# Kernel optimization log

Measured on AMD Instinct MI355X. Metric: run time of the kernel, lower is better.

Reference implementation:

```python
import jax, jax.numpy as jnp
import numpy as np

D = 256      # input channels
DK = 64      # key/query/value channels
BS, W, H = 8, 64, 64


def setup_inputs() -> dict:
    key = jax.random.key(0)
    k1, k2, k3, k4 = jax.random.split(key, 4)
    v = jax.random.normal(k1, (BS, D, W, H), dtype=jnp.float32)
    # conv1x1 weights collapse to plain matrices over the channel dim
    Wqkv = jax.random.normal(k2, (3 * DK, D), dtype=jnp.float32) * 0.02
    Wout = jax.random.normal(k3, (D, DK), dtype=jnp.float32) * 0.02
    gamma = jax.random.normal(k4, (1,), dtype=jnp.float32)  # original inits to 0; nonzero for a non-degenerate baseline
    return {"v": v, "Wqkv": Wqkv, "Wout": Wout, "gamma": gamma}


def reference(v, Wqkv, Wout, gamma):
    bs, c, w, h = v.shape
    n = w * h
    d_k = Wout.shape[1]
    x = v.reshape(bs, c, n)                      # (b, c, n)
    qkv = jnp.einsum('oc,bcn->bon', Wqkv, x)      # 1x1 conv == channel matmul
    q = qkv[:, :d_k]                              # (b, dk, n)
    k = qkv[:, d_k:2 * d_k]
    val = qkv[:, 2 * d_k:]
    s = jnp.einsum('bdi,bdj->bij', q, k)          # (b, n, n) = query^T key
    beta = jax.nn.softmax(s, axis=2)              # exp(s - logsumexp(s, axis=2))
    y = jnp.einsum('bdi,bij->bdj', val, beta)     # bmm(value, beta)
    o = jnp.einsum('od,bdn->bon', Wout, y) * gamma[0] + x
    return o.reshape(bs, c, w, h)
```

## Files before the change

kernel.cpp:

```cpp
#include <hip/hip_runtime.h>

typedef unsigned short ushort_t;
typedef __bf16 bf16x8 __attribute__((ext_vector_type(8)));
typedef short short4v __attribute__((ext_vector_type(4)));
typedef float f32x4 __attribute__((ext_vector_type(4)));
typedef unsigned int uint4v __attribute__((ext_vector_type(4)));
typedef unsigned int uint2v __attribute__((ext_vector_type(2)));

#define NTOK 4096
#define DMODEL 256
#define DK 64
#define BS 8
#define LN2INV 1.44269504088896f

__device__ __forceinline__ ushort_t f2bf(float f) {
  unsigned u = __builtin_bit_cast(unsigned, f);
  u += 0x7fffu + ((u >> 16) & 1u);
  return (ushort_t)(u >> 16);
}
__device__ __forceinline__ float bf2f(ushort_t s) {
  return __builtin_bit_cast(float, ((unsigned)s) << 16);
}
__device__ __forceinline__ bf16x8 lds_frag(const ushort_t* p) {
  return __builtin_bit_cast(bf16x8, *(const uint4v*)p);
}
__device__ __forceinline__ float fexp2(float x) {
#if __has_builtin(__builtin_amdgcn_exp2f)
  return __builtin_amdgcn_exp2f(x);
#else
  return exp2f(x);
#endif
}
__device__ __forceinline__ unsigned bfpack(float x, float y) {
  return __builtin_amdgcn_perm(__builtin_bit_cast(unsigned, y),
                               __builtin_bit_cast(unsigned, x), 0x07060302u);
}
__device__ __forceinline__ f32x4 mfma16(short4v a, short4v b, f32x4 c) {
#if defined(__HIP_DEVICE_COMPILE__)
#if __has_builtin(__builtin_amdgcn_mfma_f32_16x16x16bf16_1k)
  return __builtin_amdgcn_mfma_f32_16x16x16bf16_1k(a, b, c, 0, 0, 0);
#else
  typedef __bf16 bf16x4 __attribute__((ext_vector_type(4)));
  return __builtin_amdgcn_mfma_f32_16x16x16_bf16(__builtin_bit_cast(bf16x4, a),
                                                 __builtin_bit_cast(bf16x4, b), c, 0, 0, 0);
#endif
#else
  (void)a; (void)b;
  return c;
#endif
}

__global__ __launch_bounds__(256) void k_convert(const float* __restrict__ Wqkv,
                                                 const float* __restrict__ Wout,
                                                 ushort_t* __restrict__ Wb,
                                                 ushort_t* __restrict__ Woutb) {
  int i = blockIdx.x * 256 + threadIdx.x;
  if (i < 3 * DK * DMODEL) {
    float w = Wqkv[i];
    if (i < DK * DMODEL) w *= LN2INV;
    Wb[i] = f2bf(w);
  } else {
    int j = i - 3 * DK * DMODEL;
    Woutb[j] = f2bf(Wout[j]);
  }
}

__global__ __launch_bounds__(256) void k_transpose(const float* __restrict__ x,
                                                   ushort_t* __restrict__ xT) {
  const int b = blockIdx.z;
  const int c0 = blockIdx.y * 64;
  const int n0 = blockIdx.x * 64;
  const int tid = threadIdx.x;
  __shared__ __align__(16) ushort_t t[64 * 72];
  const float* xb = x + (size_t)b * DMODEL * NTOK;
  ushort_t* xTb = xT + (size_t)b * NTOK * DMODEL;
#pragma unroll
  for (int kr = 0; kr < 2; kr++) {
    int s = tid + 256 * kr;
    int c = s >> 3, ns = (s & 7) * 8;
    const float* src = xb + (size_t)(c0 + c) * NTOK + n0 + ns;
    f32x4 a = *(const f32x4*)src;
    f32x4 bq = *(const f32x4*)(src + 4);
    uint4v o;
    o.x = (unsigned)f2bf(a[0]) | ((unsigned)f2bf(a[1]) << 16);
    o.y = (unsigned)f2bf(a[2]) | ((unsigned)f2bf(a[3]) << 16);
    o.z = (unsigned)f2bf(bq[0]) | ((unsigned)f2bf(bq[1]) << 16);
    o.w = (unsigned)f2bf(bq[2]) | ((unsigned)f2bf(bq[3]) << 16);
    *(uint4v*)(t + c * 72 + ns) = o;
  }
  __syncthreads();
#pragma unroll
  for (int kr = 0; kr < 2; kr++) {
    int s = tid + 256 * kr;
    int n = s >> 3, cs = (s & 7) * 8;
    unsigned e0 = t[(cs + 0) * 72 + n], e1 = t[(cs + 1) * 72 + n];
    unsigned e2 = t[(cs + 2) * 72 + n], e3 = t[(cs + 3) * 72 + n];
    unsigned e4 = t[(cs + 4) * 72 + n], e5 = t[(cs + 5) * 72 + n];
    unsigned e6 = t[(cs + 6) * 72 + n], e7 = t[(cs + 7) * 72 + n];
    uint4v o;
    o.x = e0 | (e1 << 16); o.y = e2 | (e3 << 16);
    o.z = e4 | (e5 << 16); o.w = e6 | (e7 << 16);
    *(uint4v*)(xTb + (size_t)(n0 + n) * DMODEL + c0 + cs) = o;
  }
}

__global__ __launch_bounds__(256) void k_qkv(const ushort_t* __restrict__ xT,
                                             const ushort_t* __restrict__ W,
                                             ushort_t* __restrict__ QT,
                                             ushort_t* __restrict__ KT,
                                             ushort_t* __restrict__ Vv) {
  const int b = blockIdx.y;
  const int n0 = blockIdx.x * 64;
  const int tid = threadIdx.x;
  const int lane = tid & 63, wv = tid >> 6;
  const int quad = lane >> 4, l15 = lane & 15;
  __shared__ __align__(16) ushort_t lw[192 * 40];
  __shared__ __align__(16) ushort_t lx[64 * 40];
  f32x4 acc[3][4];
  const f32x4 zero4 = {0.f, 0.f, 0.f, 0.f};
#pragma unroll
  for (int i = 0; i < 3; i++)
#pragma unroll
    for (int j = 0; j < 4; j++) acc[i][j] = zero4;

  const ushort_t* xTb = xT + ((size_t)b * NTOK + n0) * DMODEL;

  for (int c0 = 0; c0 < DMODEL; c0 += 32) {
    __syncthreads();
#pragma unroll
    for (int kr = 0; kr < 3; kr++) {
      int s = tid + 256 * kr;
      int o = s >> 2, cs = (s & 3) * 8;
      *(uint4v*)(lw + o * 40 + cs) = *(const uint4v*)(W + o * DMODEL + c0 + cs);
    }
    {
      int n = tid >> 2, cs = (tid & 3) * 8;
      *(uint4v*)(lx + n * 40 + cs) = *(const uint4v*)(xTb + (size_t)n * DMODEL + c0 + cs);
    }
    __syncthreads();
    bf16x8 bb[4];
#pragma unroll
    for (int nt = 0; nt < 4; nt++) bb[nt] = lds_frag(lx + (nt * 16 + l15) * 40 + quad * 8);
#pragma unroll
    for (int mt = 0; mt < 3; mt++) {
      bf16x8 a = lds_frag(lw + (wv * 48 + mt * 16 + l15) * 40 + quad * 8);
#pragma unroll
      for (int nt = 0; nt < 4; nt++)
        acc[mt][nt] = __builtin_amdgcn_mfma_f32_16x16x32_bf16(a, bb[nt], acc[mt][nt], 0, 0, 0);
    }
  }
#pragma unroll
  for (int mt = 0; mt < 3; mt++) {
    int o = wv * 48 + mt * 16 + quad * 4;
#pragma unroll
    for (int nt = 0; nt < 4; nt++) {
      int n = n0 + nt * 16 + l15;
      f32x4 v4 = acc[mt][nt];
      if (o < 128) {
        ushort_t* dst = (o < 64) ? (QT + ((size_t)b * NTOK + n) * DK + o)
                                 : (KT + ((size_t)b * NTOK + n) * DK + (o - 64));
        uint2v ww;
        ww.x = (unsigned)f2bf(v4[0]) | ((unsigned)f2bf(v4[1]) << 16);
        ww.y = (unsigned)f2bf(v4[2]) | ((unsigned)f2bf(v4[3]) << 16);
        *(uint2v*)dst = ww;
      } else {
        int d = o - 128;
#pragma unroll
        for (int r = 0; r < 4; r++)
          Vv[((size_t)b * DK + d + r) * NTOK + n] = f2bf(v4[r]);
      }
    }
  }
}

__global__ __launch_bounds__(256) void k_rsum(const ushort_t* __restrict__ QT,
                                              const ushort_t* __restrict__ KT,
                                              float* __restrict__ Rp) {
  const int id = blockIdx.x;
  const int b = id & 7;
  const int rest = id >> 3;
  const int i0 = (rest & 63) * 64;
  const int jh = rest >> 6;
  const int tid = threadIdx.x;
  const int lane = tid & 63, wv = tid >> 6;
  const int quad = lane >> 4, l15 = lane & 15;
  __shared__ __align__(16) ushort_t lq[64 * 72];
  __shared__ __align__(16) ushort_t lk[2][64 * 72];
  const ushort_t* QTb = QT + ((size_t)b * NTOK + i0) * DK;
  const ushort_t* KTb = KT + ((size_t)b * NTOK + jh * 2048) * DK;
#pragma unroll
  for (int kr = 0; kr < 2; kr++) {
    int s = tid + 256 * kr;
    int row = s >> 3, ds = (s & 7) * 8;
    *(uint4v*)(lq + row * 72 + ds) = *(const uint4v*)(QTb + (size_t)row * DK + ds);
    *(uint4v*)(lk[0] + row * 72 + ds) = *(const uint4v*)(KTb + (size_t)row * DK + ds);
  }
  __syncthreads();
  bf16x8 a0 = lds_frag(lq + (wv * 16 + l15) * 72 + quad * 8);
  bf16x8 a1 = lds_frag(lq + (wv * 16 + l15) * 72 + 32 + quad * 8);
  float lsum0 = 0.f, lsum1 = 0.f, lsum2 = 0.f, lsum3 = 0.f;
  const f32x4 zero4 = {0.f, 0.f, 0.f, 0.f};
  for (int it = 0; it < 32; it++) {
    if (it + 1 < 32) {
      const ushort_t* src = KTb + (size_t)(it + 1) * 64 * DK;
      ushort_t* dstb = lk[(it + 1) & 1];
#pragma unroll
      for (int kr = 0; kr < 2; kr++) {
        int s = tid + 256 * kr;
        int row = s >> 3, ds = (s & 7) * 8;
        *(uint4v*)(dstb + row * 72 + ds) = *(const uint4v*)(src + (size_t)row * DK + ds);
      }
    }
    const ushort_t* kb = lk[it & 1];
#pragma unroll
    for (int nt = 0; nt < 4; nt++) {
      bf16x8 b0 = lds_frag(kb + (nt * 16 + l15) * 72 + quad * 8);
      bf16x8 b1 = lds_frag(kb + (nt * 16 + l15) * 72 + 32 + quad * 8);
      f32x4 s4 = __builtin_amdgcn_mfma_f32_16x16x32_bf16(a0, b0, zero4, 0, 0, 0);
      s4 = __builtin_amdgcn_mfma_f32_16x16x32_bf16(a1, b1, s4, 0, 0, 0);
      lsum0 += fexp2(s4[0]);
      lsum1 += fexp2(s4[1]);
      lsum2 += fexp2(s4[2]);
      lsum3 += fexp2(s4[3]);
    }
    __syncthreads();
  }
#pragma unroll
  for (int off = 1; off < 16; off <<= 1) {
    lsum0 += __shfl_xor(lsum0, off);
    lsum1 += __shfl_xor(lsum1, off);
    lsum2 += __shfl_xor(lsum2, off);
    lsum3 += __shfl_xor(lsum3, off);
  }
  if (l15 < 4) {
    float v = (l15 == 0) ? lsum0 : (l15 == 1) ? lsum1 : (l15 == 2) ? lsum2 : lsum3;
    Rp[((size_t)(jh * 8 + b)) * NTOK + i0 + wv * 16 + quad * 4 + l15] = v;
  }
}

__global__ __launch_bounds__(256) void k_rmerge(const float* __restrict__ Rp,
                                                float* __restrict__ Rr) {
  int g = blockIdx.x * 256 + threadIdx.x;
  Rr[g] = 1.0f / (Rp[g] + Rp[BS * NTOK + g]);
}

__global__ __launch_bounds__(256) void k_pv(const ushort_t* __restrict__ QT,
                                            const ushort_t* __restrict__ KT,
                                            const ushort_t* __restrict__ Vv,
                                            const float* __restrict__ Rr,
                                            ushort_t* __restrict__ Yp) {
  const int id = blockIdx.x;
  const int b = id & 7;
  const int rest = id >> 3;
  const int j0 = (rest & 63) * 64;
  const int ih = rest >> 6;
  const int tid = threadIdx.x;
  const int lane = tid & 63, wv = tid >> 6;
  const int quad = lane >> 4, l15 = lane & 15;

  __shared__ __align__(16) ushort_t pool[18432];
#define LQ(buf) (pool + (buf) * 4608)
#define LV(buf) (pool + 9216 + (buf) * 4608)
  float* rbuf = (float*)pool;
  ushort_t* pbuf = pool + 8704;

  const ushort_t* KTb = KT + ((size_t)b * NTOK + j0) * DK;
  const ushort_t* QTb = QT + ((size_t)b * NTOK + ih * 2048) * DK;
  const ushort_t* Vbb = Vv + (size_t)b * DK * NTOK + ih * 2048;
  const float* Rrb = Rr + (size_t)b * NTOK + ih * 2048;

#pragma unroll
  for (int kr = 0; kr < 2; kr++) {
    int s = tid + 256 * kr;
    int row = s >> 3, ds = (s & 7) * 8;
    *(uint4v*)(LQ(0) + row * 72 + ds) = *(const uint4v*)(KTb + (size_t)row * DK + ds);
  }
  __syncthreads();
  bf16x8 kb0[4], kb1[4];
#pragma unroll
  for (int nt = 0; nt < 4; nt++) {
    kb0[nt] = lds_frag(LQ(0) + (nt * 16 + l15) * 72 + quad * 8);
    kb1[nt] = lds_frag(LQ(0) + (nt * 16 + l15) * 72 + 32 + quad * 8);
  }
  __syncthreads();
#pragma unroll
  for (int kr = 0; kr < 2; kr++) {
    int s = tid + 256 * kr;
    int row = s >> 3, ds = (s & 7) * 8;
    *(uint4v*)(LQ(0) + row * 72 + ds) = *(const uint4v*)(QTb + (size_t)row * DK + ds);
    *(uint4v*)(LV(0) + row * 72 + ds) = *(const uint4v*)(Vbb + (size_t)row * NTOK + ds);
  }
  __syncthreads();

  const f32x4 zero4 = {0.f, 0.f, 0.f, 0.f};
  f32x4 yt[4][4];
#pragma unroll
  for (int i = 0; i < 4; i++)
#pragma unroll
    for (int j = 0; j < 4; j++) yt[i][j] = zero4;

  for (int it = 0; it < 32; it++) {
    const int cb = it & 1, nb = cb ^ 1;
    f32x4 rv = *(const f32x4*)(Rrb + it * 64 + wv * 16 + quad * 4);
    if (it + 1 < 32) {
      const ushort_t* qsrc = QTb + (size_t)(it + 1) * 64 * DK;
#pragma unroll
      for (int kr = 0; kr < 2; kr++) {
        int s = tid + 256 * kr;
        int row = s >> 3, ds = (s & 7) * 8;
        *(uint4v*)(LQ(nb) + row * 72 + ds) = *(const uint4v*)(qsrc + (size_t)row * DK + ds);
        *(uint4v*)(LV(nb) + row * 72 + ds) =
            *(const uint4v*)(Vbb + (size_t)row * NTOK + (it + 1) * 64 + ds);
      }
    }
    bf16x8 a0 = lds_frag(LQ(cb) + (wv * 16 + l15) * 72 + quad * 8);
    bf16x8 a1 = lds_frag(LQ(cb) + (wv * 16 + l15) * 72 + 32 + quad * 8);
    short4v vf[4];
#pragma unroll
    for (int dsub = 0; dsub < 4; dsub++)
      vf[dsub] = __builtin_bit_cast(short4v,
          *(const uint2v*)(LV(cb) + (dsub * 16 + l15) * 72 + wv * 16 + quad * 4));
#pragma unroll
    for (int nt = 0; nt < 4; nt++) {
      f32x4 s4 = __builtin_amdgcn_mfma_f32_16x16x32_bf16(a0, kb0[nt], zero4, 0, 0, 0);
      s4 = __builtin_amdgcn_mfma_f32_16x16x32_bf16(a1, kb1[nt], s4, 0, 0, 0);
      uint2v wp;
      wp.x = bfpack(fexp2(s4[0]) * rv[0], fexp2(s4[1]) * rv[1]);
      wp.y = bfpack(fexp2(s4[2]) * rv[2], fexp2(s4[3]) * rv[3]);
      short4v wf = __builtin_bit_cast(short4v, wp);
#pragma unroll
      for (int dsub = 0; dsub < 4; dsub++)
        yt[nt][dsub] = mfma16(wf, vf[dsub], yt[nt][dsub]);
    }
    __syncthreads();
  }

  if (wv == 0) {
#pragma unroll
    for (int nt = 0; nt < 4; nt++)
#pragma unroll
      for (int dsub = 0; dsub < 4; dsub++)
        *(f32x4*)(rbuf + (dsub * 16 + l15) * 68 + nt * 16 + quad * 4) = yt[nt][dsub];
  }
  __syncthreads();
  if (wv == 1) {
#pragma unroll
    for (int nt = 0; nt < 4; nt++)
#pragma unroll
      for (int dsub = 0; dsub < 4; dsub++) {
        float* p = rbuf + (dsub * 16 + l15) * 68 + nt * 16 + quad * 4;
        *(f32x4*)p = *(const f32x4*)p + yt[nt][dsub];
      }
  }
  __syncthreads();
  if (wv == 2) {
#pragma unroll
    for (int nt = 0; nt < 4; nt++)
#pragma unroll
      for (int dsub = 0; dsub < 4; dsub++) {
        float* p = rbuf + (dsub * 16 + l15) * 68 + nt * 16 + quad * 4;
        *(f32x4*)p = *(const f32x4*)p + yt[nt][dsub];
      }
  }
  __syncthreads();
  if (wv == 3) {
#pragma unroll
    for (int nt = 0; nt < 4; nt++)
#pragma unroll
      for (int dsub = 0; dsub < 4; dsub++) {
        const float* p = rbuf + (dsub * 16 + l15) * 68 + nt * 16 + quad * 4;
        f32x4 v4 = *(const f32x4*)p + yt[nt][dsub];
#pragma unroll
        for (int r = 0; r < 4; r++)
          pbuf[(nt * 16 + quad * 4 + r) * 72 + dsub * 16 + l15] = f2bf(v4[r]);
      }
  }
  __syncthreads();

  ushort_t* Ypb = Yp + ((size_t)(ih * 8 + b) * NTOK + j0) * DK;
#pragma unroll
  for (int kr = 0; kr < 2; kr++) {
    int s = tid + 256 * kr;
    int row = s >> 3, c8 = (s & 7) * 8;
    *(uint4v*)(Ypb + (size_t)row * DK + c8) = *(const uint4v*)(pbuf + row * 72 + c8);
  }
#undef LQ
#undef LV
}

__global__ __launch_bounds__(256) void k_out(const ushort_t* __restrict__ Yp,
                                             const ushort_t* __restrict__ Wout,
                                             const float* __restrict__ gammap,
                                             const float* __restrict__ x,
                                             float* __restrict__ outp) {
  const int id = blockIdx.x;
  const int b = id & 7;
  const int n0 = (id >> 3) * 64;
  const int tid = threadIdx.x;
  const int lane = tid & 63, wv = tid >> 6;
  const int quad = lane >> 4, l15 = lane & 15;
  __shared__ __align__(16) ushort_t pbuf[64 * 72];

  const ushort_t* Y0 = Yp + ((size_t)b * NTOK + n0) * DK;
  const ushort_t* Y1 = Yp + ((size_t)(8 + b) * NTOK + n0) * DK;
#pragma unroll
  for (int kr = 0; kr < 2; kr++) {
    int s = tid + 256 * kr;
    int row = s >> 3, c8 = (s & 7) * 8;
    uint4v ua = *(const uint4v*)(Y0 + (size_t)row * DK + c8);
    uint4v ub = *(const uint4v*)(Y1 + (size_t)row * DK + c8);
    uint4v oc;
    unsigned* pa = (unsigned*)&ua;
    unsigned* pb = (unsigned*)&ub;
    unsigned* po = (unsigned*)&oc;
#pragma unroll
    for (int w = 0; w < 4; w++) {
      float lo = bf2f((ushort_t)(pa[w] & 0xffff)) + bf2f((ushort_t)(pb[w] & 0xffff));
      float hi = bf2f((ushort_t)(pa[w] >> 16)) + bf2f((ushort_t)(pb[w] >> 16));
      po[w] = bfpack(lo, hi);
    }
    *(uint4v*)(pbuf + row * 72 + c8) = oc;
  }
  __syncthreads();

  const f32x4 zero4 = {0.f, 0.f, 0.f, 0.f};
  bf16x8 yb0[4], yb1[4];
#pragma unroll
  for (int nt = 0; nt < 4; nt++) {
    yb0[nt] = lds_frag(pbuf + (nt * 16 + l15) * 72 + quad * 8);
    yb1[nt] = lds_frag(pbuf + (nt * 16 + l15) * 72 + 32 + quad * 8);
  }
  f32x4 oacc[4][4];
#pragma unroll
  for (int m = 0; m < 4; m++)
#pragma unroll
    for (int nt = 0; nt < 4; nt++) oacc[m][nt] = zero4;
#pragma unroll
  for (int m = 0; m < 4; m++) {
    int c = (wv * 4 + m) * 16 + l15;
    bf16x8 aw0 = __builtin_bit_cast(bf16x8, *(const uint4v*)(Wout + c * DK + quad * 8));
    bf16x8 aw1 = __builtin_bit_cast(bf16x8, *(const uint4v*)(Wout + c * DK + 32 + quad * 8));
#pragma unroll
    for (int nt = 0; nt < 4; nt++) {
      oacc[m][nt] = __builtin_amdgcn_mfma_f32_16x16x32_bf16(aw0, yb0[nt], oacc[m][nt], 0, 0, 0);
      oacc[m][nt] = __builtin_amdgcn_mfma_f32_16x16x32_bf16(aw1, yb1[nt], oacc[m][nt], 0, 0, 0);
    }
  }
  float g = gammap[0];
  const float* xb = x + (size_t)b * DMODEL * NTOK;
  float* ob = outp + (size_t)b * DMODEL * NTOK;
#pragma unroll
  for (int m = 0; m < 4; m++) {
    int cbase = (wv * 4 + m) * 16 + quad * 4;
#pragma unroll
    for (int nt = 0; nt < 4; nt++) {
      int n = n0 + nt * 16 + l15;
#pragma unroll
      for (int r = 0; r < 4; r++) {
        size_t idx = (size_t)(cbase + r) * NTOK + n;
        ob[idx] = oacc[m][nt][r] * g + xb[idx];
      }
    }
  }
}

extern "C" void kernel_launch(void* const* d_in, const int* in_sizes, int n_in,
                              void* d_out, int out_size, void* d_ws, size_t ws_size,
                              hipStream_t stream) {
  const float* v = (const float*)d_in[0];
  const float* Wqkv = (const float*)d_in[1];
  const float* Wout = (const float*)d_in[2];
  const float* gamma = (const float*)d_in[3];
  float* outp = (float*)d_out;

  ushort_t* xT = (ushort_t*)d_ws;
  ushort_t* QT = xT + (size_t)BS * NTOK * DMODEL;
  ushort_t* KT = QT + (size_t)BS * NTOK * DK;
  ushort_t* Vs = KT + (size_t)BS * NTOK * DK;
  ushort_t* Wb = Vs + (size_t)BS * DK * NTOK;
  ushort_t* Woutb = Wb + 3 * DK * DMODEL;
  float* Rp = (float*)(Woutb + DMODEL * DK);
  float* Rr = Rp + 2 * (size_t)BS * NTOK;
  ushort_t* Yp = (ushort_t*)(Rr + (size_t)BS * NTOK);

  k_convert<<<dim3(256), 256, 0, stream>>>(Wqkv, Wout, Wb, Woutb);
  k_transpose<<<dim3(64, 4, BS), 256, 0, stream>>>(v, xT);
  k_qkv<<<dim3(64, BS), 256, 0, stream>>>(xT, Wb, QT, KT, Vs);
  k_rsum<<<dim3(1024), 256, 0, stream>>>(QT, KT, Rp);
  k_rmerge<<<dim3(128), 256, 0, stream>>>(Rp, Rr);
  k_pv<<<dim3(1024), 256, 0, stream>>>(QT, KT, Vs, Rr, Yp);
  k_out<<<dim3(512), 256, 0, stream>>>(Yp, Woutb, gamma, v, outp);
}
```

Measured before the change: 217.4 us.

## Load MFMA fragments directly from global memory and fold normalizer into exponent

The rsum and pv kernels stop staging Q, K and V tiles through LDS and instead load MFMA operand fragments straight from global memory into registers, double-buffered across iterations. This removes the per-iteration __syncthreads barriers and the LDS round trips. The merge kernel now stores -log2 of the row sum, and pv feeds it in as the MFMA accumulator init, so the normalization folds into the exp2 argument and the per-element multiply goes away. The cost is more register pressure and global loads that are less coalesced and repeated across waves, served mostly from cache.

```diff
diff --git a/kernel.cpp b/kernel.cpp
--- a/kernel.cpp
+++ b/kernel.cpp
@@ -23,6 +23,12 @@
 }
 __device__ __forceinline__ bf16x8 lds_frag(const ushort_t* p) {
   return __builtin_bit_cast(bf16x8, *(const uint4v*)p);
+}
+__device__ __forceinline__ bf16x8 ldg8(const ushort_t* p) {
+  return __builtin_bit_cast(bf16x8, *(const uint4v*)p);
+}
+__device__ __forceinline__ short4v ldg4(const ushort_t* p) {
+  return __builtin_bit_cast(short4v, *(const uint2v*)p);
 }
 __device__ __forceinline__ float fexp2(float x) {
 #if __has_builtin(__builtin_amdgcn_exp2f)
@@ -184,56 +190,57 @@
   const int tid = threadIdx.x;
   const int lane = tid & 63, wv = tid >> 6;
   const int quad = lane >> 4, l15 = lane & 15;
-  __shared__ __align__(16) ushort_t lq[64 * 72];
-  __shared__ __align__(16) ushort_t lk[2][64 * 72];
   const ushort_t* QTb = QT + ((size_t)b * NTOK + i0) * DK;
   const ushort_t* KTb = KT + ((size_t)b * NTOK + jh * 2048) * DK;
-#pragma unroll
-  for (int kr = 0; kr < 2; kr++) {
-    int s = tid + 256 * kr;
-    int row = s >> 3, ds = (s & 7) * 8;
-    *(uint4v*)(lq + row * 72 + ds) = *(const uint4v*)(QTb + (size_t)row * DK + ds);
-    *(uint4v*)(lk[0] + row * 72 + ds) = *(const uint4v*)(KTb + (size_t)row * DK + ds);
-  }
-  __syncthreads();
-  bf16x8 a0 = lds_frag(lq + (wv * 16 + l15) * 72 + quad * 8);
-  bf16x8 a1 = lds_frag(lq + (wv * 16 + l15) * 72 + 32 + quad * 8);
-  float lsum0 = 0.f, lsum1 = 0.f, lsum2 = 0.f, lsum3 = 0.f;
+
+  const int qoff = (wv * 16 + l15) * DK + quad * 8;
+  bf16x8 a0 = ldg8(QTb + qoff);
+  bf16x8 a1 = ldg8(QTb + qoff + 32);
+
+  const int koff = l15 * DK + quad * 8;
+  bf16x8 kb0[2][4], kb1[2][4];
+  float ls0 = 0.f, ls1 = 0.f, ls2 = 0.f, ls3 = 0.f;
   const f32x4 zero4 = {0.f, 0.f, 0.f, 0.f};
-  for (int it = 0; it < 32; it++) {
-    if (it + 1 < 32) {
-      const ushort_t* src = KTb + (size_t)(it + 1) * 64 * DK;
-      ushort_t* dstb = lk[(it + 1) & 1];
-#pragma unroll
-      for (int kr = 0; kr < 2; kr++) {
-        int s = tid + 256 * kr;
-        int row = s >> 3, ds = (s & 7) * 8;
-        *(uint4v*)(dstb + row * 72 + ds) = *(const uint4v*)(src + (size_t)row * DK + ds);
-      }
-    }
-    const ushort_t* kb = lk[it & 1];
-#pragma unroll
-    for (int nt = 0; nt < 4; nt++) {
-      bf16x8 b0 = lds_frag(kb + (nt * 16 + l15) * 72 + quad * 8);
-      bf16x8 b1 = lds_frag(kb + (nt * 16 + l15) * 72 + 32 + quad * 8);
-      f32x4 s4 = __builtin_amdgcn_mfma_f32_16x16x32_bf16(a0, b0, zero4, 0, 0, 0);
-      s4 = __builtin_amdgcn_mfma_f32_16x16x32_bf16(a1, b1, s4, 0, 0, 0);
-      lsum0 += fexp2(s4[0]);
-      lsum1 += fexp2(s4[1]);
-      lsum2 += fexp2(s4[2]);
-      lsum3 += fexp2(s4[3]);
-    }
-    __syncthreads();
-  }
+
+#define LOADK(bb, itv)                                                       \
+  {                                                                          \
+    _Pragma("unroll") for (int nt = 0; nt < 4; nt++) {                       \
+      const ushort_t* kp = KTb + (size_t)((itv)*64 + nt * 16) * DK + koff;   \
+      kb0[bb][nt] = ldg8(kp);                                                \
+      kb1[bb][nt] = ldg8(kp + 32);                                           \
+    }                                                                        \
+  }
+#define STEPK(bb)                                                            \
+  {                                                                          \
+    _Pragma("unroll") for (int nt = 0; nt < 4; nt++) {                       \
+      f32x4 s4 = __builtin_amdgcn_mfma_f32_16x16x32_bf16(a0, kb0[bb][nt], zero4, 0, 0, 0); \
+      s4 = __builtin_amdgcn_mfma_f32_16x16x32_bf16(a1, kb1[bb][nt], s4, 0, 0, 0);          \
+      ls0 += fexp2(s4[0]);                                                   \
+      ls1 += fexp2(s4[1]);                                                   \
+      ls2 += fexp2(s4[2]);                                                   \
+      ls3 += fexp2(s4[3]);                                                   \
+    }                                                                        \
+  }
+
+  LOADK(0, 0);
+  for (int it = 0; it < 32; it += 2) {
+    LOADK(1, it + 1);
+    STEPK(0);
+    if (it + 2 < 32) LOADK(0, it + 2);
+    STEPK(1);
+  }
+#undef LOADK
+#undef STEPK
+
 #pragma unroll
   for (int off = 1; off < 16; off <<= 1) {
-    lsum0 += __shfl_xor(lsum0, off);
-    lsum1 += __shfl_xor(lsum1, off);
-    lsum2 += __shfl_xor(lsum2, off);
-    lsum3 += __shfl_xor(lsum3, off);
+    ls0 += __shfl_xor(ls0, off);
+    ls1 += __shfl_xor(ls1, off);
+    ls2 += __shfl_xor(ls2, off);
+    ls3 += __shfl_xor(ls3, off);
   }
   if (l15 < 4) {
-    float v = (l15 == 0) ? lsum0 : (l15 == 1) ? lsum1 : (l15 == 2) ? lsum2 : lsum3;
+    float v = (l15 == 0) ? ls0 : (l15 == 1) ? ls1 : (l15 == 2) ? ls2 : ls3;
     Rp[((size_t)(jh * 8 + b)) * NTOK + i0 + wv * 16 + quad * 4 + l15] = v;
   }
 }
@@ -241,7 +248,8 @@
 __global__ __launch_bounds__(256) void k_rmerge(const float* __restrict__ Rp,
                                                 float* __restrict__ Rr) {
   int g = blockIdx.x * 256 + threadIdx.x;
-  Rr[g] = 1.0f / (Rp[g] + Rp[BS * NTOK + g]);
+  float s = Rp[g] + Rp[BS * NTOK + g];
+  Rr[g] = -__log2f(s);
 }
 
 __global__ __launch_bounds__(256) void k_pv(const ushort_t* __restrict__ QT,
@@ -258,9 +266,7 @@
   const int lane = tid & 63, wv = tid >> 6;
   const int quad = lane >> 4, l15 = lane & 15;
 
-  __shared__ __align__(16) ushort_t pool[18432];
-#define LQ(buf) (pool + (buf) * 4608)
-#define LV(buf) (pool + 9216 + (buf) * 4608)
+  __shared__ __align__(16) ushort_t pool[13312];
   float* rbuf = (float*)pool;
   ushort_t* pbuf = pool + 8704;
 
@@ -269,71 +275,60 @@
   const ushort_t* Vbb = Vv + (size_t)b * DK * NTOK + ih * 2048;
   const float* Rrb = Rr + (size_t)b * NTOK + ih * 2048;
 
-#pragma unroll
-  for (int kr = 0; kr < 2; kr++) {
-    int s = tid + 256 * kr;
-    int row = s >> 3, ds = (s & 7) * 8;
-    *(uint4v*)(LQ(0) + row * 72 + ds) = *(const uint4v*)(KTb + (size_t)row * DK + ds);
-  }
-  __syncthreads();
   bf16x8 kb0[4], kb1[4];
 #pragma unroll
   for (int nt = 0; nt < 4; nt++) {
-    kb0[nt] = lds_frag(LQ(0) + (nt * 16 + l15) * 72 + quad * 8);
-    kb1[nt] = lds_frag(LQ(0) + (nt * 16 + l15) * 72 + 32 + quad * 8);
-  }
-  __syncthreads();
-#pragma unroll
-  for (int kr = 0; kr < 2; kr++) {
-    int s = tid + 256 * kr;
-    int row = s >> 3, ds = (s & 7) * 8;
-    *(uint4v*)(LQ(0) + row * 72 + ds) = *(const uint4v*)(QTb + (size_t)row * DK + ds);
-    *(uint4v*)(LV(0) + row * 72 + ds) = *(const uint4v*)(Vbb + (size_t)row * NTOK + ds);
-  }
-  __syncthreads();
-
+    const ushort_t* kp = KTb + (size_t)(nt * 16 + l15) * DK + quad * 8;
+    kb0[nt] = ldg8(kp);
+    kb1[nt] = ldg8(kp + 32);
+  }
+
+  f32x4 yt[4][4];
   const f32x4 zero4 = {0.f, 0.f, 0.f, 0.f};
-  f32x4 yt[4][4];
 #pragma unroll
   for (int i = 0; i < 4; i++)
 #pragma unroll
     for (int j = 0; j < 4; j++) yt[i][j] = zero4;
 
-  for (int it = 0; it < 32; it++) {
-    const int cb = it & 1, nb = cb ^ 1;
-    f32x4 rv = *(const f32x4*)(Rrb + it * 64 + wv * 16 + quad * 4);
-    if (it + 1 < 32) {
-      const ushort_t* qsrc = QTb + (size_t)(it + 1) * 64 * DK;
-#pragma unroll
-      for (int kr = 0; kr < 2; kr++) {
-        int s = tid + 256 * kr;
-        int row = s >> 3, ds = (s & 7) * 8;
-        *(uint4v*)(LQ(nb) + row * 72 + ds) = *(const uint4v*)(qsrc + (size_t)row * DK + ds);
-        *(uint4v*)(LV(nb) + row * 72 + ds) =
-            *(const uint4v*)(Vbb + (size_t)row * NTOK + (it + 1) * 64 + ds);
-      }
-    }
-    bf16x8 a0 = lds_frag(LQ(cb) + (wv * 16 + l15) * 72 + quad * 8);
-    bf16x8 a1 = lds_frag(LQ(cb) + (wv * 16 + l15) * 72 + 32 + quad * 8);
-    short4v vf[4];
-#pragma unroll
-    for (int dsub = 0; dsub < 4; dsub++)
-      vf[dsub] = __builtin_bit_cast(short4v,
-          *(const uint2v*)(LV(cb) + (dsub * 16 + l15) * 72 + wv * 16 + quad * 4));
-#pragma unroll
-    for (int nt = 0; nt < 4; nt++) {
-      f32x4 s4 = __builtin_amdgcn_mfma_f32_16x16x32_bf16(a0, kb0[nt], zero4, 0, 0, 0);
-      s4 = __builtin_amdgcn_mfma_f32_16x16x32_bf16(a1, kb1[nt], s4, 0, 0, 0);
-      uint2v wp;
-      wp.x = bfpack(fexp2(s4[0]) * rv[0], fexp2(s4[1]) * rv[1]);
-      wp.y = bfpack(fexp2(s4[2]) * rv[2], fexp2(s4[3]) * rv[3]);
-      short4v wf = __builtin_bit_cast(short4v, wp);
-#pragma unroll
-      for (int dsub = 0; dsub < 4; dsub++)
-        yt[nt][dsub] = mfma16(wf, vf[dsub], yt[nt][dsub]);
-    }
-    __syncthreads();
-  }
+  const int qoff = (wv * 16 + l15) * DK + quad * 8;
+  const int voff = wv * 16 + quad * 4;
+
+  bf16x8 qa0[2], qa1[2];
+  short4v vf[2][4];
+  f32x4 lr[2];
+
+#define LOADT(bb, itv)                                                        \
+  {                                                                           \
+    const ushort_t* qp = QTb + (size_t)(itv)*64 * DK + qoff;                  \
+    qa0[bb] = ldg8(qp);                                                       \
+    qa1[bb] = ldg8(qp + 32);                                                  \
+    lr[bb] = *(const f32x4*)(Rrb + (itv)*64 + voff);                          \
+    _Pragma("unroll") for (int ds = 0; ds < 4; ds++)                          \
+        vf[bb][ds] = ldg4(Vbb + (size_t)(ds * 16 + l15) * NTOK + (itv)*64 + voff); \
+  }
+#define STEPT(bb)                                                             \
+  {                                                                           \
+    _Pragma("unroll") for (int nt = 0; nt < 4; nt++) {                        \
+      f32x4 s4 = __builtin_amdgcn_mfma_f32_16x16x32_bf16(qa0[bb], kb0[nt], lr[bb], 0, 0, 0); \
+      s4 = __builtin_amdgcn_mfma_f32_16x16x32_bf16(qa1[bb], kb1[nt], s4, 0, 0, 0);           \
+      uint2v wp;                                                              \
+      wp.x = bfpack(fexp2(s4[0]), fexp2(s4[1]));                              \
+      wp.y = bfpack(fexp2(s4[2]), fexp2(s4[3]));                              \
+      short4v wf = __builtin_bit_cast(short4v, wp);                           \
+      _Pragma("unroll") for (int ds = 0; ds < 4; ds++)                        \
+          yt[nt][ds] = mfma16(wf, vf[bb][ds], yt[nt][ds]);                    \
+    }                                                                         \
+  }
+
+  LOADT(0, 0);
+  for (int it = 0; it < 32; it += 2) {
+    LOADT(1, it + 1);
+    STEPT(0);
+    if (it + 2 < 32) LOADT(0, it + 2);
+    STEPT(1);
+  }
+#undef LOADT
+#undef STEPT
 
   if (wv == 0) {
 #pragma unroll
@@ -384,8 +379,6 @@
     int row = s >> 3, c8 = (s & 7) * 8;
     *(uint4v*)(Ypb + (size_t)row * DK + c8) = *(const uint4v*)(pbuf + row * 72 + c8);
   }
-#undef LQ
-#undef LV
 }
 
 __global__ __launch_bounds__(256) void k_out(const ushort_t* __restrict__ Yp,
```

After: 338.0 us. 1.55x slower.

## Register-stage global prefetch, load fragments directly, fold softmax normalizer into MFMA bias

Applied to the files above, without the earlier changes.

The double-buffered tile prefetch in the row-sum and PV kernels now loads into registers before the MFMA work and writes them to LDS only after it, so global latency overlaps compute rather than stalling on a direct global-to-LDS store. Q fragments in k_rsum and K fragments in k_pv are read straight from global memory, which drops an LDS round trip and a barrier. The reciprocal row sum becomes -log2(sum) and is passed as the MFMA accumulator's initial value, replacing four multiplies per score tile with a free add inside exp2. This adds register pressure for the staged values and assumes fragment rows match the per-row bias layout.

```diff
diff --git a/kernel.cpp b/kernel.cpp
--- a/kernel.cpp
+++ b/kernel.cpp
@@ -184,32 +184,30 @@
   const int tid = threadIdx.x;
   const int lane = tid & 63, wv = tid >> 6;
   const int quad = lane >> 4, l15 = lane & 15;
-  __shared__ __align__(16) ushort_t lq[64 * 72];
   __shared__ __align__(16) ushort_t lk[2][64 * 72];
   const ushort_t* QTb = QT + ((size_t)b * NTOK + i0) * DK;
   const ushort_t* KTb = KT + ((size_t)b * NTOK + jh * 2048) * DK;
-#pragma unroll
-  for (int kr = 0; kr < 2; kr++) {
-    int s = tid + 256 * kr;
-    int row = s >> 3, ds = (s & 7) * 8;
-    *(uint4v*)(lq + row * 72 + ds) = *(const uint4v*)(QTb + (size_t)row * DK + ds);
-    *(uint4v*)(lk[0] + row * 72 + ds) = *(const uint4v*)(KTb + (size_t)row * DK + ds);
-  }
-  __syncthreads();
-  bf16x8 a0 = lds_frag(lq + (wv * 16 + l15) * 72 + quad * 8);
-  bf16x8 a1 = lds_frag(lq + (wv * 16 + l15) * 72 + 32 + quad * 8);
-  float lsum0 = 0.f, lsum1 = 0.f, lsum2 = 0.f, lsum3 = 0.f;
+
+  const int qoff = (wv * 16 + l15) * DK + quad * 8;
+  bf16x8 a0 = __builtin_bit_cast(bf16x8, *(const uint4v*)(QTb + qoff));
+  bf16x8 a1 = __builtin_bit_cast(bf16x8, *(const uint4v*)(QTb + qoff + 32));
+
+  const int sr0 = tid >> 3, sr1 = sr0 + 32;
+  const int c8 = (tid & 7) * 8;
+
+  *(uint4v*)(lk[0] + sr0 * 72 + c8) = *(const uint4v*)(KTb + (size_t)sr0 * DK + c8);
+  *(uint4v*)(lk[0] + sr1 * 72 + c8) = *(const uint4v*)(KTb + (size_t)sr1 * DK + c8);
+  __syncthreads();
+
+  float ls0 = 0.f, ls1 = 0.f, ls2 = 0.f, ls3 = 0.f;
   const f32x4 zero4 = {0.f, 0.f, 0.f, 0.f};
+
   for (int it = 0; it < 32; it++) {
+    uint4v p0, p1;
     if (it + 1 < 32) {
       const ushort_t* src = KTb + (size_t)(it + 1) * 64 * DK;
-      ushort_t* dstb = lk[(it + 1) & 1];
-#pragma unroll
-      for (int kr = 0; kr < 2; kr++) {
-        int s = tid + 256 * kr;
-        int row = s >> 3, ds = (s & 7) * 8;
-        *(uint4v*)(dstb + row * 72 + ds) = *(const uint4v*)(src + (size_t)row * DK + ds);
-      }
+      p0 = *(const uint4v*)(src + (size_t)sr0 * DK + c8);
+      p1 = *(const uint4v*)(src + (size_t)sr1 * DK + c8);
     }
     const ushort_t* kb = lk[it & 1];
 #pragma unroll
@@ -218,22 +216,28 @@
       bf16x8 b1 = lds_frag(kb + (nt * 16 + l15) * 72 + 32 + quad * 8);
       f32x4 s4 = __builtin_amdgcn_mfma_f32_16x16x32_bf16(a0, b0, zero4, 0, 0, 0);
       s4 = __builtin_amdgcn_mfma_f32_16x16x32_bf16(a1, b1, s4, 0, 0, 0);
-      lsum0 += fexp2(s4[0]);
-      lsum1 += fexp2(s4[1]);
-      lsum2 += fexp2(s4[2]);
-      lsum3 += fexp2(s4[3]);
+      ls0 += fexp2(s4[0]);
+      ls1 += fexp2(s4[1]);
+      ls2 += fexp2(s4[2]);
+      ls3 += fexp2(s4[3]);
+    }
+    if (it + 1 < 32) {
+      ushort_t* dstb = lk[(it + 1) & 1];
+      *(uint4v*)(dstb + sr0 * 72 + c8) = p0;
+      *(uint4v*)(dstb + sr1 * 72 + c8) = p1;
     }
     __syncthreads();
   }
+
 #pragma unroll
   for (int off = 1; off < 16; off <<= 1) {
-    lsum0 += __shfl_xor(lsum0, off);
-    lsum1 += __shfl_xor(lsum1, off);
-    lsum2 += __shfl_xor(lsum2, off);
-    lsum3 += __shfl_xor(lsum3, off);
+    ls0 += __shfl_xor(ls0, off);
+    ls1 += __shfl_xor(ls1, off);
+    ls2 += __shfl_xor(ls2, off);
+    ls3 += __shfl_xor(ls3, off);
   }
   if (l15 < 4) {
-    float v = (l15 == 0) ? lsum0 : (l15 == 1) ? lsum1 : (l15 == 2) ? lsum2 : lsum3;
+    float v = (l15 == 0) ? ls0 : (l15 == 1) ? ls1 : (l15 == 2) ? ls2 : ls3;
     Rp[((size_t)(jh * 8 + b)) * NTOK + i0 + wv * 16 + quad * 4 + l15] = v;
   }
 }
@@ -241,7 +245,8 @@
 __global__ __launch_bounds__(256) void k_rmerge(const float* __restrict__ Rp,
                                                 float* __restrict__ Rr) {
   int g = blockIdx.x * 256 + threadIdx.x;
-  Rr[g] = 1.0f / (Rp[g] + Rp[BS * NTOK + g]);
+  float s = Rp[g] + Rp[BS * NTOK + g];
+  Rr[g] = -__log2f(s);
 }
 
 __global__ __launch_bounds__(256) void k_pv(const ushort_t* __restrict__ QT,
@@ -269,31 +274,25 @@
   const ushort_t* Vbb = Vv + (size_t)b * DK * NTOK + ih * 2048;
   const float* Rrb = Rr + (size_t)b * NTOK + ih * 2048;
 
-#pragma unroll
-  for (int kr = 0; kr < 2; kr++) {
-    int s = tid + 256 * kr;
-    int row = s >> 3, ds = (s & 7) * 8;
-    *(uint4v*)(LQ(0) + row * 72 + ds) = *(const uint4v*)(KTb + (size_t)row * DK + ds);
-  }
-  __syncthreads();
   bf16x8 kb0[4], kb1[4];
 #pragma unroll
   for (int nt = 0; nt < 4; nt++) {
-    kb0[nt] = lds_frag(LQ(0) + (nt * 16 + l15) * 72 + quad * 8);
-    kb1[nt] = lds_frag(LQ(0) + (nt * 16 + l15) * 72 + 32 + quad * 8);
-  }
-  __syncthreads();
-#pragma unroll
-  for (int kr = 0; kr < 2; kr++) {
-    int s = tid + 256 * kr;
-    int row = s >> 3, ds = (s & 7) * 8;
-    *(uint4v*)(LQ(0) + row * 72 + ds) = *(const uint4v*)(QTb + (size_t)row * DK + ds);
-    *(uint4v*)(LV(0) + row * 72 + ds) = *(const uint4v*)(Vbb + (size_t)row * NTOK + ds);
-  }
-  __syncthreads();
-
+    const ushort_t* kp = KTb + (size_t)(nt * 16 + l15) * DK + quad * 8;
+    kb0[nt] = __builtin_bit_cast(bf16x8, *(const uint4v*)kp);
+    kb1[nt] = __builtin_bit_cast(bf16x8, *(const uint4v*)(kp + 32));
+  }
+
+  const int sr0 = tid >> 3, sr1 = sr0 + 32;
+  const int c8 = (tid & 7) * 8;
+
+  *(uint4v*)(LQ(0) + sr0 * 72 + c8) = *(const uint4v*)(QTb + (size_t)sr0 * DK + c8);
+  *(uint4v*)(LQ(0) + sr1 * 72 + c8) = *(const uint4v*)(QTb + (size_t)sr1 * DK + c8);
+  *(uint4v*)(LV(0) + sr0 * 72 + c8) = *(const uint4v*)(Vbb + (size_t)sr0 * NTOK + c8);
+  *(uint4v*)(LV(0) + sr1 * 72 + c8) = *(const uint4v*)(Vbb + (size_t)sr1 * NTOK + c8);
+  __syncthreads();
+
+  f32x4 yt[4][4];
   const f32x4 zero4 = {0.f, 0.f, 0.f, 0.f};
-  f32x4 yt[4][4];
 #pragma unroll
   for (int i = 0; i < 4; i++)
 #pragma unroll
@@ -301,17 +300,14 @@
 
   for (int it = 0; it < 32; it++) {
     const int cb = it & 1, nb = cb ^ 1;
-    f32x4 rv = *(const f32x4*)(Rrb + it * 64 + wv * 16 + quad * 4);
+    f32x4 lrv = *(const f32x4*)(Rrb + it * 64 + wv * 16 + quad * 4);
+    uint4v q0, q1, v0, v1;
     if (it + 1 < 32) {
       const ushort_t* qsrc = QTb + (size_t)(it + 1) * 64 * DK;
-#pragma unroll
-      for (int kr = 0; kr < 2; kr++) {
-        int s = tid + 256 * kr;
-        int row = s >> 3, ds = (s & 7) * 8;
-        *(uint4v*)(LQ(nb) + row * 72 + ds) = *(const uint4v*)(qsrc + (size_t)row * DK + ds);
-        *(uint4v*)(LV(nb) + row * 72 + ds) =
-            *(const uint4v*)(Vbb + (size_t)row * NTOK + (it + 1) * 64 + ds);
-      }
+      q0 = *(const uint4v*)(qsrc + (size_t)sr0 * DK + c8);
+      q1 = *(const uint4v*)(qsrc + (size_t)sr1 * DK + c8);
+      v0 = *(const uint4v*)(Vbb + (size_t)sr0 * NTOK + (it + 1) * 64 + c8);
+      v1 = *(const uint4v*)(Vbb + (size_t)sr1 * NTOK + (it + 1) * 64 + c8);
     }
     bf16x8 a0 = lds_frag(LQ(cb) + (wv * 16 + l15) * 72 + quad * 8);
     bf16x8 a1 = lds_frag(LQ(cb) + (wv * 16 + l15) * 72 + 32 + quad * 8);
@@ -322,15 +318,21 @@
           *(const uint2v*)(LV(cb) + (dsub * 16 + l15) * 72 + wv * 16 + quad * 4));
 #pragma unroll
     for (int nt = 0; nt < 4; nt++) {
-      f32x4 s4 = __builtin_amdgcn_mfma_f32_16x16x32_bf16(a0, kb0[nt], zero4, 0, 0, 0);
+      f32x4 s4 = __builtin_amdgcn_mfma_f32_16x16x32_bf16(a0, kb0[nt], lrv, 0, 0, 0);
       s4 = __builtin_amdgcn_mfma_f32_16x16x32_bf16(a1, kb1[nt], s4, 0, 0, 0);
       uint2v wp;
-      wp.x = bfpack(fexp2(s4[0]) * rv[0], fexp2(s4[1]) * rv[1]);
-      wp.y = bfpack(fexp2(s4[2]) * rv[2], fexp2(s4[3]) * rv[3]);
+      wp.x = bfpack(fexp2(s4[0]), fexp2(s4[1]));
+      wp.y = bfpack(fexp2(s4[2]), fexp2(s4[3]));
       short4v wf = __builtin_bit_cast(short4v, wp);
 #pragma unroll
       for (int dsub = 0; dsub < 4; dsub++)
         yt[nt][dsub] = mfma16(wf, vf[dsub], yt[nt][dsub]);
+    }
+    if (it + 1 < 32) {
+      *(uint4v*)(LQ(nb) + sr0 * 72 + c8) = q0;
+      *(uint4v*)(LQ(nb) + sr1 * 72 + c8) = q1;
+      *(uint4v*)(LV(nb) + sr0 * 72 + c8) = v0;
+      *(uint4v*)(LV(nb) + sr1 * 72 + c8) = v1;
     }
     __syncthreads();
   }
@@ -381,8 +383,8 @@
 #pragma unroll
   for (int kr = 0; kr < 2; kr++) {
     int s = tid + 256 * kr;
-    int row = s >> 3, c8 = (s & 7) * 8;
-    *(uint4v*)(Ypb + (size_t)row * DK + c8) = *(const uint4v*)(pbuf + row * 72 + c8);
+    int row = s >> 3, cc = (s & 7) * 8;
+    *(uint4v*)(Ypb + (size_t)row * DK + cc) = *(const uint4v*)(pbuf + row * 72 + cc);
   }
 #undef LQ
 #undef LV
```

Measured after the change: 220.5 us. About the same (+1.4%).
